# Performance work log

Measured on AMD Instinct MI355X. Metric: run time of the kernel, lower is better.

## Reference

```python
import jax, jax.numpy as jnp
import jax.lax as lax
import numpy as np

G = 128    # number of asset groups (batch)
A = 100    # n_assets per group
WIN = 10   # window_size
FD = 16    # feature_dim
H = 128    # hidden_dim


def setup_inputs() -> dict:
    key = jax.random.key(0)
    ks = jax.random.split(key, 12)
    N = G * A
    def glorot(k, shape, fan_in):
        return (jax.random.normal(k, shape, jnp.float32) / np.sqrt(fan_in)).astype(jnp.float32)
    return {
        "x": jax.random.normal(ks[0], (N, WIN, FD), jnp.float32),
        "W1": glorot(ks[1], (WIN * FD, H), WIN * FD),
        "b1": jnp.zeros((H,), jnp.float32),
        "W2": glorot(ks[2], (H, H), H),
        "b2": jnp.zeros((H,), jnp.float32),
        "W3": glorot(ks[3], (H, H), H),
        "b3": jnp.zeros((H,), jnp.float32),
        "cw1": glorot(ks[4], (H, 1, 1, 3), 3),      # conv2d_1 weight [out,in,kh,kw]
        "cb1": jnp.zeros((H,), jnp.float32),
        "cw2": glorot(ks[5], (1, H, 1, 3), 3 * H),  # conv2d_2 weight
        "cb2": jnp.zeros((1,), jnp.float32),
    }


def _corrcoef(r):
    xc = r - r.mean(axis=1, keepdims=True)
    cov = xc @ xc.T                      # divisor cancels in correlation
    d = jnp.sqrt(jnp.diag(cov))
    return cov / (d[:, None] * d[None, :])


def _conv1x3(h, w, b):
    # h: [1,C,N,H]; kernel (1,3), padding (0,1) -> NCHW conv
    out = lax.conv_general_dilated(h, w, (1, 1), ((0, 0), (1, 1)),
                                   dimension_numbers=("NCHW", "OIHW", "NCHW"))
    return out + b[None, :, None, None]


def reference(x, W1, b1, W2, b2, W3, b3, cw1, cb1, cw2, cb2):
    # block-diagonal adjacency == independent per-group adjacencies
    returns = x[:, :, -1].reshape(G, A, WIN)
    corr = jax.vmap(_corrcoef)(returns)                  # [G,A,A]
    adj = 1.0 - jnp.abs(corr) + jnp.eye(A, dtype=x.dtype)
    dinv = 1.0 / jnp.sqrt(adj.sum(axis=-1))              # [G,A]
    norm_adj = dinv[:, :, None] * adj * dinv[:, None, :] # D^-1/2 A D^-1/2

    feats = x.reshape(G, A, WIN * FD)
    h = jax.nn.relu(jnp.einsum("gij,gjf->gif", norm_adj, feats) @ W1 + b1)
    h = jax.nn.relu(jnp.einsum("gij,gjh->gih", norm_adj, h) @ W2 + b2)
    h = jax.nn.relu(jnp.einsum("gij,gjh->gih", norm_adj, h) @ W3 + b3)

    h = h.reshape(1, 1, G * A, H)                        # [1,1,N,H]
    h = jax.nn.relu(_conv1x3(h, cw1, cb1))               # [1,H,N,H]
    out = _conv1x3(h, cw2, cb2)                          # [1,1,N,H]
    return out[0, 0]                                     # [N,H]
```

## Files before the change

kernel.cpp:

```cpp
#include <hip/hip_runtime.h>

#define G   128
#define A   100
#define WIN 10
#define FD  16
#define H   128
#define NROWS (G*A)
#define K1  (WIN*FD)

typedef __attribute__((ext_vector_type(8))) short short8;
typedef __attribute__((ext_vector_type(4))) short short4v;
typedef __attribute__((ext_vector_type(4))) float floatx4;

struct BfPair { short h, l; };

__device__ inline unsigned short f2bf(float f) {
    unsigned u = __float_as_uint(f);
    u += 0x7fff + ((u >> 16) & 1);
    return (unsigned short)(u >> 16);
}
__device__ inline float bf2f(unsigned short h) {
    return __uint_as_float(((unsigned)h) << 16);
}
__device__ inline BfPair split1(float v) {
    BfPair p;
    unsigned short hb = f2bf(v);
    p.h = (short)hb;
    p.l = (short)f2bf(v - bf2f(hb));
    return p;
}

__global__ __launch_bounds__(256) void k_prep(const float* __restrict__ W1,
                                              const float* __restrict__ W2,
                                              const float* __restrict__ W3,
                                              const float* __restrict__ cw1,
                                              const float* __restrict__ cb1,
                                              const float* __restrict__ cw2,
                                              const float* __restrict__ cb2,
                                              short* __restrict__ Wh,
                                              short* __restrict__ Wl,
                                              float* __restrict__ wpack) {
    const int b = blockIdx.x, t = threadIdx.x;
    if (b < 26) {
        int l, kc, K;
        const float* Wsrc;
        if (b < 10)      { l = 0; kc = b;      K = K1; Wsrc = W1; }
        else if (b < 18) { l = 1; kc = b - 10; K = H;  Wsrc = W2; }
        else             { l = 2; kc = b - 18; K = H;  Wsrc = W3; }
        short* dh = Wh + l * 128 * 160;
        short* dl = Wl + l * 128 * 160;
        for (int e = t; e < 16 * 128; e += 256) {
            int k = kc * 16 + (e >> 7), n = e & 127;
            BfPair p = split1(Wsrc[(size_t)k * H + n]);
            dh[n * 160 + k] = p.h;
            dl[n * 160 + k] = p.l;
        }
        (void)K;
    } else {
        for (int e = t; e < 1024; e += 256) {
            int c = e >> 3, s = e & 7;
            float v;
            if (s < 3)       v = cw1[3 * c + s];
            else if (s == 3) v = cb1[c];
            else if (s < 7)  v = cw2[3 * c + (s - 4)];
            else             v = cb2[0];
            wpack[e] = v;
        }
    }
}

__global__ __launch_bounds__(256) void k_nadj(const float* __restrict__ x,
                                              short* __restrict__ Sh,
                                              short* __restrict__ Sl) {
    __shared__ float xcT[WIN][104];
    __shared__ float invn[A];
    __shared__ float adjs[A][101];
    __shared__ float dinv[A];
    const int g = blockIdx.x;
    const int t = threadIdx.x;

    for (int idx = t; idx < A * WIN; idx += 256) {
        int a = idx / WIN, w = idx % WIN;
        xcT[w][a] = x[((g * A + a) * WIN + w) * FD + (FD - 1)];
    }
    __syncthreads();
    if (t < A) {
        float m = 0.f;
        #pragma unroll
        for (int w = 0; w < WIN; w++) m += xcT[w][t];
        m *= (1.0f / WIN);
        float ss = 0.f;
        #pragma unroll
        for (int w = 0; w < WIN; w++) {
            float v = xcT[w][t] - m;
            xcT[w][t] = v;
            ss += v * v;
        }
        invn[t] = rsqrtf(ss);
    }
    __syncthreads();
    for (int tt2 = t; tt2 < 2500; tt2 += 256) {
        int ti = tt2 / 50, tj = tt2 % 50;
        int i0 = 2 * ti, j0v = 2 * tj;
        float d00 = 0.f, d01 = 0.f, d10 = 0.f, d11 = 0.f;
        #pragma unroll
        for (int w = 0; w < WIN; w++) {
            float2 xi = *(const float2*)&xcT[w][i0];
            float2 xj = *(const float2*)&xcT[w][j0v];
            d00 = fmaf(xi.x, xj.x, d00); d01 = fmaf(xi.x, xj.y, d01);
            d10 = fmaf(xi.y, xj.x, d10); d11 = fmaf(xi.y, xj.y, d11);
        }
        float ii0 = invn[i0], ii1 = invn[i0 + 1];
        float ij0 = invn[j0v], ij1 = invn[j0v + 1];
        float e = (ti == tj) ? 1.f : 0.f;
        adjs[i0][j0v]         = 1.f - fabsf(d00 * ii0 * ij0) + e;
        adjs[i0][j0v + 1]     = 1.f - fabsf(d01 * ii0 * ij1);
        adjs[i0 + 1][j0v]     = 1.f - fabsf(d10 * ii1 * ij0);
        adjs[i0 + 1][j0v + 1] = 1.f - fabsf(d11 * ii1 * ij1) + e;
    }
    __syncthreads();
    if (t < A) {
        float s = 0.f;
        for (int j = 0; j < A; j++) s += adjs[t][j];
        dinv[t] = rsqrtf(s);
    }
    __syncthreads();
    short* sh = Sh + (size_t)g * 112 * 128;
    short* sl = Sl + (size_t)g * 112 * 128;
    for (int idx = t; idx < 112 * 128; idx += 256) {
        int i = idx >> 7, k = idx & 127;
        float v = (i < A && k < A) ? dinv[i] * adjs[i][k] * dinv[k] : 0.f;
        BfPair p = split1(v);
        sh[idx] = p.h;
        sl[idx] = p.l;
    }
}

__global__ __launch_bounds__(256) void k_layer(const short* __restrict__ Sh,
                                               const short* __restrict__ Sl,
                                               const short* __restrict__ Whg,
                                               const short* __restrict__ Wlg,
                                               const float* __restrict__ X,
                                               const float* __restrict__ bias,
                                               float* __restrict__ Z, int K) {
    __shared__ short Xh[112 * 40], Xl[112 * 40];
    __shared__ short Yh[32 * 136], Yl[32 * 136];
    const int g = blockIdx.x;
    const int cbase = blockIdx.y * 32;
    const int t = threadIdx.x;
    const int w = t >> 6, lane = t & 63;
    const int quad = lane >> 4, r16 = lane & 15;
    const int nm = (w < 3) ? 2 : 1;
    const int m0 = 2 * w;

    for (int e = t; e < 384; e += 256) {
        int r = 100 + e / 32, c = e % 32;
        Xh[r * 40 + c] = 0; Xl[r * 40 + c] = 0;
    }
    for (int e = t; e < 512; e += 256) {
        int n = e >> 4, k = 112 + (e & 15);
        Yh[n * 136 + k] = 0; Yl[n * 136 + k] = 0;
    }

    floatx4 acc[2][2];
    #pragma unroll
    for (int i = 0; i < 2; i++)
        #pragma unroll
        for (int j = 0; j < 2; j++) acc[i][j] = (floatx4)0.f;

    const float* Xg = X + (size_t)g * A * K;
    const int nch = K >> 5;
    for (int c = 0; c < nch; c++) {
        const int k0 = c << 5;
        __syncthreads();
        for (int e = t; e < 400; e += 256) {
            int r = e >> 2, q = e & 3;
            const float* gp = Xg + (size_t)r * K + k0 + q * 8;
            float4 f0 = *(const float4*)gp;
            float4 f1 = *(const float4*)(gp + 4);
            float v[8] = {f0.x, f0.y, f0.z, f0.w, f1.x, f1.y, f1.z, f1.w};
            short8 hh, ll;
            #pragma unroll
            for (int i = 0; i < 8; i++) {
                BfPair p = split1(v[i]);
                hh[i] = p.h; ll[i] = p.l;
            }
            *(short8*)&Xh[r * 40 + q * 8] = hh;
            *(short8*)&Xl[r * 40 + q * 8] = ll;
        }
        __syncthreads();
        short8 bh[2], bl[2];
        #pragma unroll
        for (int nt = 0; nt < 2; nt++) {
            size_t wo = (size_t)(cbase + nt * 16 + r16) * 160 + k0 + quad * 8;
            bh[nt] = *(const short8*)(Whg + wo);
            bl[nt] = *(const short8*)(Wlg + wo);
        }
        for (int mt = 0; mt < nm; mt++) {
            int xo = ((m0 + mt) * 16 + r16) * 40 + quad * 8;
            short8 ah = *(const short8*)&Xh[xo];
            short8 al = *(const short8*)&Xl[xo];
            #pragma unroll
            for (int nt = 0; nt < 2; nt++) {
                acc[mt][nt] = __builtin_amdgcn_mfma_f32_16x16x32_bf16(ah, bh[nt], acc[mt][nt], 0, 0, 0);
                acc[mt][nt] = __builtin_amdgcn_mfma_f32_16x16x32_bf16(ah, bl[nt], acc[mt][nt], 0, 0, 0);
                acc[mt][nt] = __builtin_amdgcn_mfma_f32_16x16x32_bf16(al, bh[nt], acc[mt][nt], 0, 0, 0);
            }
        }
    }
    __syncthreads();

    for (int mt = 0; mt < nm; mt++) {
        #pragma unroll
        for (int nt = 0; nt < 2; nt++) {
            short4v yh4, yl4;
            #pragma unroll
            for (int rr = 0; rr < 4; rr++) {
                BfPair p = split1(acc[mt][nt][rr]);
                yh4[rr] = p.h; yl4[rr] = p.l;
            }
            int off = (nt * 16 + r16) * 136 + (m0 + mt) * 16 + quad * 4;
            *(short4v*)&Yh[off] = yh4;
            *(short4v*)&Yl[off] = yl4;
            acc[mt][nt] = (floatx4)0.f;
        }
    }
    __syncthreads();

    const short* Sgh = Sh + (size_t)g * 112 * 128;
    const short* Sgl = Sl + (size_t)g * 112 * 128;
    #pragma unroll
    for (int c = 0; c < 4; c++) {
        const int k0 = c << 5;
        short8 bh[2], bl[2];
        #pragma unroll
        for (int nt = 0; nt < 2; nt++) {
            int yo = (nt * 16 + r16) * 136 + k0 + quad * 8;
            bh[nt] = *(const short8*)&Yh[yo];
            bl[nt] = *(const short8*)&Yl[yo];
        }
        for (int mt = 0; mt < nm; mt++) {
            size_t so = (size_t)((m0 + mt) * 16 + r16) * 128 + k0 + quad * 8;
            short8 ah = *(const short8*)(Sgh + so);
            short8 al = *(const short8*)(Sgl + so);
            #pragma unroll
            for (int nt = 0; nt < 2; nt++) {
                acc[mt][nt] = __builtin_amdgcn_mfma_f32_16x16x32_bf16(ah, bh[nt], acc[mt][nt], 0, 0, 0);
                acc[mt][nt] = __builtin_amdgcn_mfma_f32_16x16x32_bf16(ah, bl[nt], acc[mt][nt], 0, 0, 0);
                acc[mt][nt] = __builtin_amdgcn_mfma_f32_16x16x32_bf16(al, bh[nt], acc[mt][nt], 0, 0, 0);
            }
        }
    }

    #pragma unroll
    for (int nt = 0; nt < 2; nt++) {
        float bv = bias[cbase + nt * 16 + r16];
        for (int mt = 0; mt < nm; mt++) {
            #pragma unroll
            for (int rr = 0; rr < 4; rr++) {
                int i = (m0 + mt) * 16 + quad * 4 + rr;
                if (i < A)
                    Z[((size_t)g * A + i) * H + cbase + nt * 16 + r16] =
                        fmaxf(0.f, acc[mt][nt][rr] + bv);
            }
        }
    }
}

__global__ __launch_bounds__(256) void k_conv(const float* __restrict__ h3,
                                              const float* __restrict__ wpack,
                                              float* __restrict__ out) {
    const int t = threadIdx.x;
    const int wave = t >> 6, lane = t & 63;
    const int n = blockIdx.x * 8 + wave * 2 + (lane >> 5);
    const int q = lane & 31;
    const int j0 = q * 4;
    const float* hr = h3 + (size_t)n * H;

    float hh[8];
    if (q == 0) {
        float4 a  = *(const float4*)(hr);
        float2 b2 = *(const float2*)(hr + 4);
        hh[0] = 0.f;  hh[1] = 0.f;  hh[2] = a.x;  hh[3] = a.y;
        hh[4] = a.z;  hh[5] = a.w;  hh[6] = b2.x; hh[7] = b2.y;
    } else if (q == 31) {
        float2 b2 = *(const float2*)(hr + 122);
        float4 a  = *(const float4*)(hr + 124);
        hh[0] = b2.x; hh[1] = b2.y; hh[2] = a.x;  hh[3] = a.y;
        hh[4] = a.z;  hh[5] = a.w;  hh[6] = 0.f;  hh[7] = 0.f;
    } else {
        float4 a  = *(const float4*)(hr + j0 - 2);
        float4 b4 = *(const float4*)(hr + j0 + 2);
        hh[0] = a.x;  hh[1] = a.y;  hh[2] = a.z;  hh[3] = a.w;
        hh[4] = b4.x; hh[5] = b4.y; hh[6] = b4.z; hh[7] = b4.w;
    }
    const float mlo = (q == 0)  ? 0.f : 1.f;
    const float mhi = (q == 31) ? 0.f : 1.f;

    float acc[4] = {0.f, 0.f, 0.f, 0.f};
    #pragma unroll 8
    for (int c = 0; c < H; c++) {
        const float* wp = wpack + c * 8;
        float w0 = wp[0], w1 = wp[1], w2 = wp[2], b = wp[3];
        float v0 = wp[4], v1 = wp[5], v2 = wp[6];
        float tt[6];
        #pragma unroll
        for (int m = 0; m < 6; m++)
            tt[m] = fmaxf(0.f, fmaf(w2, hh[m + 2],
                               fmaf(w1, hh[m + 1],
                               fmaf(w0, hh[m], b))));
        tt[0] *= mlo;
        tt[5] *= mhi;
        #pragma unroll
        for (int p = 0; p < 4; p++)
            acc[p] = fmaf(v0, tt[p],
                     fmaf(v1, tt[p + 1],
                     fmaf(v2, tt[p + 2], acc[p])));
    }
    const float c2b = wpack[7];
    *(float4*)(out + (size_t)n * H + j0) =
        make_float4(acc[0] + c2b, acc[1] + c2b, acc[2] + c2b, acc[3] + c2b);
}

extern "C" void kernel_launch(void* const* d_in, const int* in_sizes, int n_in,
                              void* d_out, int out_size, void* d_ws, size_t ws_size,
                              hipStream_t stream) {
    const float* x   = (const float*)d_in[0];
    const float* W1  = (const float*)d_in[1];
    const float* b1  = (const float*)d_in[2];
    const float* W2  = (const float*)d_in[3];
    const float* b2  = (const float*)d_in[4];
    const float* W3  = (const float*)d_in[5];
    const float* b3  = (const float*)d_in[6];
    const float* cw1 = (const float*)d_in[7];
    const float* cb1 = (const float*)d_in[8];
    const float* cw2 = (const float*)d_in[9];
    const float* cb2 = (const float*)d_in[10];
    float* out = (float*)d_out;

    short* Sh = (short*)d_ws;
    short* Sl = Sh + (size_t)G * 112 * 128;
    short* Wh = Sl + (size_t)G * 112 * 128;
    short* Wl = Wh + 3 * 128 * 160;
    float* wpack = (float*)(Wl + 3 * 128 * 160);
    float* bufA  = wpack + 1024;
    float* bufB  = bufA + (size_t)NROWS * H;

    k_prep<<<27, 256, 0, stream>>>(W1, W2, W3, cw1, cb1, cw2, cb2, Wh, Wl, wpack);
    k_nadj<<<G, 256, 0, stream>>>(x, Sh, Sl);

    k_layer<<<dim3(G, 4), 256, 0, stream>>>(Sh, Sl, Wh,             Wl,             x,    b1, bufA, K1);
    k_layer<<<dim3(G, 4), 256, 0, stream>>>(Sh, Sl, Wh + 128 * 160, Wl + 128 * 160, bufA, b2, bufB, H);
    k_layer<<<dim3(G, 4), 256, 0, stream>>>(Sh, Sl, Wh + 256 * 160, Wl + 256 * 160, bufB, b3, bufA, H);

    k_conv<<<NROWS / 8, 256, 0, stream>>>(bufA, wpack, out);
}
```

Measured before the change: 200.6 us.

## Split GCN layer into global X@W and S@Y kernels with bf16-pair intermediates

Each fused per-group layer kernel becomes two kernels. k_ymm computes X@W over 16-row tiles across all groups and writes transposed Y as bf16 hi/lo into a padded per-group buffer. k_smm then multiplies the normalized adjacency by Y and applies bias and ReLU, storing bf16 hi/lo (fp32 on the last layer). The aim is to stop recomputing the X tile split for every column block, to avoid LDS round trips and barriers, and to store intermediates in a smaller bf16 form. The conv kernel now stages its weights in LDS itself and handles two rows per thread, and the wpack prep path is gone. The cost is more kernel launches, 64-thread blocks with lower occupancy per block, and scattered 2-byte global stores of Y.

```diff
diff --git a/kernel.cpp b/kernel.cpp
--- a/kernel.cpp
+++ b/kernel.cpp
@@ -9,7 +9,6 @@
 #define K1  (WIN*FD)
 
 typedef __attribute__((ext_vector_type(8))) short short8;
-typedef __attribute__((ext_vector_type(4))) short short4v;
 typedef __attribute__((ext_vector_type(4))) float floatx4;
 
 struct BfPair { short h, l; };
@@ -33,51 +32,46 @@
 __global__ __launch_bounds__(256) void k_prep(const float* __restrict__ W1,
                                               const float* __restrict__ W2,
                                               const float* __restrict__ W3,
-                                              const float* __restrict__ cw1,
-                                              const float* __restrict__ cb1,
-                                              const float* __restrict__ cw2,
-                                              const float* __restrict__ cb2,
                                               short* __restrict__ Wh,
-                                              short* __restrict__ Wl,
-                                              float* __restrict__ wpack) {
+                                              short* __restrict__ Wl) {
     const int b = blockIdx.x, t = threadIdx.x;
-    if (b < 26) {
-        int l, kc, K;
-        const float* Wsrc;
-        if (b < 10)      { l = 0; kc = b;      K = K1; Wsrc = W1; }
-        else if (b < 18) { l = 1; kc = b - 10; K = H;  Wsrc = W2; }
-        else             { l = 2; kc = b - 18; K = H;  Wsrc = W3; }
-        short* dh = Wh + l * 128 * 160;
-        short* dl = Wl + l * 128 * 160;
-        for (int e = t; e < 16 * 128; e += 256) {
-            int k = kc * 16 + (e >> 7), n = e & 127;
-            BfPair p = split1(Wsrc[(size_t)k * H + n]);
-            dh[n * 160 + k] = p.h;
-            dl[n * 160 + k] = p.l;
-        }
-        (void)K;
-    } else {
-        for (int e = t; e < 1024; e += 256) {
-            int c = e >> 3, s = e & 7;
-            float v;
-            if (s < 3)       v = cw1[3 * c + s];
-            else if (s == 3) v = cb1[c];
-            else if (s < 7)  v = cw2[3 * c + (s - 4)];
-            else             v = cb2[0];
-            wpack[e] = v;
-        }
+    int l, kc;
+    const float* Wsrc;
+    if (b < 10)      { l = 0; kc = b;      Wsrc = W1; }
+    else if (b < 18) { l = 1; kc = b - 10; Wsrc = W2; }
+    else             { l = 2; kc = b - 18; Wsrc = W3; }
+    short* dh = Wh + l * 128 * 160;
+    short* dl = Wl + l * 128 * 160;
+    for (int e = t; e < 16 * 128; e += 256) {
+        int k = kc * 16 + (e >> 7), n = e & 127;
+        BfPair p = split1(Wsrc[(size_t)k * H + n]);
+        dh[n * 160 + k] = p.h;
+        dl[n * 160 + k] = p.l;
     }
 }
 
 __global__ __launch_bounds__(256) void k_nadj(const float* __restrict__ x,
                                               short* __restrict__ Sh,
-                                              short* __restrict__ Sl) {
+                                              short* __restrict__ Sl,
+                                              short* __restrict__ Yh,
+                                              short* __restrict__ Yl) {
     __shared__ float xcT[WIN][104];
     __shared__ float invn[A];
     __shared__ float adjs[A][101];
     __shared__ float dinv[A];
     const int g = blockIdx.x;
     const int t = threadIdx.x;
+
+    {
+        short8 z8 = (short8)0;
+        short* ygh = Yh + (size_t)g * 128 * 128;
+        short* ygl = Yl + (size_t)g * 128 * 128;
+        for (int e = t; e < 512; e += 256) {
+            int n = e >> 2, j = 96 + (e & 3) * 8;
+            *(short8*)(ygh + n * 128 + j) = z8;
+            *(short8*)(ygl + n * 128 + j) = z8;
+        }
+    }
 
     for (int idx = t; idx < A * WIN; idx += 256) {
         int a = idx / WIN, w = idx % WIN;
@@ -136,148 +130,129 @@
     }
 }
 
-__global__ __launch_bounds__(256) void k_layer(const short* __restrict__ Sh,
-                                               const short* __restrict__ Sl,
-                                               const short* __restrict__ Whg,
-                                               const short* __restrict__ Wlg,
-                                               const float* __restrict__ X,
-                                               const float* __restrict__ bias,
-                                               float* __restrict__ Z, int K) {
-    __shared__ short Xh[112 * 40], Xl[112 * 40];
-    __shared__ short Yh[32 * 136], Yl[32 * 136];
-    const int g = blockIdx.x;
-    const int cbase = blockIdx.y * 32;
-    const int t = threadIdx.x;
-    const int w = t >> 6, lane = t & 63;
-    const int quad = lane >> 4, r16 = lane & 15;
-    const int nm = (w < 3) ? 2 : 1;
-    const int m0 = 2 * w;
-
-    for (int e = t; e < 384; e += 256) {
-        int r = 100 + e / 32, c = e % 32;
-        Xh[r * 40 + c] = 0; Xl[r * 40 + c] = 0;
-    }
-    for (int e = t; e < 512; e += 256) {
-        int n = e >> 4, k = 112 + (e & 15);
-        Yh[n * 136 + k] = 0; Yl[n * 136 + k] = 0;
-    }
-
-    floatx4 acc[2][2];
-    #pragma unroll
-    for (int i = 0; i < 2; i++)
-        #pragma unroll
-        for (int j = 0; j < 2; j++) acc[i][j] = (floatx4)0.f;
-
-    const float* Xg = X + (size_t)g * A * K;
+__global__ __launch_bounds__(64) void k_ymm(const float* __restrict__ X1,
+                                            const short* __restrict__ Zh,
+                                            const short* __restrict__ Zl,
+                                            const short* __restrict__ Whg,
+                                            const short* __restrict__ Wlg,
+                                            short* __restrict__ Yh,
+                                            short* __restrict__ Yl, int K) {
+    const int mtile = blockIdx.x;
+    const int lane = threadIdx.x;
+    const int r16 = lane & 15, quad = lane >> 4;
+    const int row = mtile * 16 + r16;
+
+    floatx4 acc[8];
+    #pragma unroll
+    for (int nt = 0; nt < 8; nt++) acc[nt] = (floatx4)0.f;
+
     const int nch = K >> 5;
     for (int c = 0; c < nch; c++) {
         const int k0 = c << 5;
-        __syncthreads();
-        for (int e = t; e < 400; e += 256) {
-            int r = e >> 2, q = e & 3;
-            const float* gp = Xg + (size_t)r * K + k0 + q * 8;
+        short8 ah, al;
+        if (K == K1) {
+            const float* gp = X1 + (size_t)row * K1 + k0 + quad * 8;
             float4 f0 = *(const float4*)gp;
             float4 f1 = *(const float4*)(gp + 4);
             float v[8] = {f0.x, f0.y, f0.z, f0.w, f1.x, f1.y, f1.z, f1.w};
-            short8 hh, ll;
             #pragma unroll
             for (int i = 0; i < 8; i++) {
                 BfPair p = split1(v[i]);
-                hh[i] = p.h; ll[i] = p.l;
+                ah[i] = p.h; al[i] = p.l;
             }
-            *(short8*)&Xh[r * 40 + q * 8] = hh;
-            *(short8*)&Xl[r * 40 + q * 8] = ll;
-        }
-        __syncthreads();
-        short8 bh[2], bl[2];
-        #pragma unroll
-        for (int nt = 0; nt < 2; nt++) {
-            size_t wo = (size_t)(cbase + nt * 16 + r16) * 160 + k0 + quad * 8;
-            bh[nt] = *(const short8*)(Whg + wo);
-            bl[nt] = *(const short8*)(Wlg + wo);
-        }
-        for (int mt = 0; mt < nm; mt++) {
-            int xo = ((m0 + mt) * 16 + r16) * 40 + quad * 8;
-            short8 ah = *(const short8*)&Xh[xo];
-            short8 al = *(const short8*)&Xl[xo];
-            #pragma unroll
-            for (int nt = 0; nt < 2; nt++) {
-                acc[mt][nt] = __builtin_amdgcn_mfma_f32_16x16x32_bf16(ah, bh[nt], acc[mt][nt], 0, 0, 0);
-                acc[mt][nt] = __builtin_amdgcn_mfma_f32_16x16x32_bf16(ah, bl[nt], acc[mt][nt], 0, 0, 0);
-                acc[mt][nt] = __builtin_amdgcn_mfma_f32_16x16x32_bf16(al, bh[nt], acc[mt][nt], 0, 0, 0);
-            }
-        }
-    }
-    __syncthreads();
-
-    for (int mt = 0; mt < nm; mt++) {
-        #pragma unroll
-        for (int nt = 0; nt < 2; nt++) {
-            short4v yh4, yl4;
-            #pragma unroll
-            for (int rr = 0; rr < 4; rr++) {
-                BfPair p = split1(acc[mt][nt][rr]);
-                yh4[rr] = p.h; yl4[rr] = p.l;
-            }
-            int off = (nt * 16 + r16) * 136 + (m0 + mt) * 16 + quad * 4;
-            *(short4v*)&Yh[off] = yh4;
-            *(short4v*)&Yl[off] = yl4;
-            acc[mt][nt] = (floatx4)0.f;
-        }
-    }
-    __syncthreads();
-
-    const short* Sgh = Sh + (size_t)g * 112 * 128;
-    const short* Sgl = Sl + (size_t)g * 112 * 128;
+        } else {
+            ah = *(const short8*)(Zh + (size_t)row * H + k0 + quad * 8);
+            al = *(const short8*)(Zl + (size_t)row * H + k0 + quad * 8);
+        }
+        #pragma unroll
+        for (int nt = 0; nt < 8; nt++) {
+            size_t wo = (size_t)(nt * 16 + r16) * 160 + k0 + quad * 8;
+            short8 bh = *(const short8*)(Whg + wo);
+            short8 bl = *(const short8*)(Wlg + wo);
+            acc[nt] = __builtin_amdgcn_mfma_f32_16x16x32_bf16(ah, bh, acc[nt], 0, 0, 0);
+            acc[nt] = __builtin_amdgcn_mfma_f32_16x16x32_bf16(ah, bl, acc[nt], 0, 0, 0);
+            acc[nt] = __builtin_amdgcn_mfma_f32_16x16x32_bf16(al, bh, acc[nt], 0, 0, 0);
+        }
+    }
+
+    #pragma unroll
+    for (int rr = 0; rr < 4; rr++) {
+        int rm = mtile * 16 + quad * 4 + rr;
+        int g = rm / 100, j = rm - g * 100;
+        size_t base = (size_t)g * 128 * 128 + j;
+        #pragma unroll
+        for (int nt = 0; nt < 8; nt++) {
+            BfPair p = split1(acc[nt][rr]);
+            size_t o = base + (size_t)(nt * 16 + r16) * 128;
+            Yh[o] = p.h;
+            Yl[o] = p.l;
+        }
+    }
+}
+
+__global__ __launch_bounds__(64) void k_smm(const short* __restrict__ Sh,
+                                            const short* __restrict__ Sl,
+                                            const short* __restrict__ Yh,
+                                            const short* __restrict__ Yl,
+                                            const float* __restrict__ bias,
+                                            short* __restrict__ Zh,
+                                            short* __restrict__ Zl,
+                                            float* __restrict__ Zf, int last) {
+    const int g = blockIdx.x, mt = blockIdx.y;
+    const int lane = threadIdx.x;
+    const int r16 = lane & 15, quad = lane >> 4;
+
+    floatx4 acc[8];
+    #pragma unroll
+    for (int nt = 0; nt < 8; nt++) acc[nt] = (floatx4)0.f;
+
+    const short* sgh = Sh + ((size_t)g * 112 + mt * 16 + r16) * 128;
+    const short* sgl = Sl + ((size_t)g * 112 + mt * 16 + r16) * 128;
+    const short* ygh = Yh + (size_t)g * 128 * 128;
+    const short* ygl = Yl + (size_t)g * 128 * 128;
+
     #pragma unroll
     for (int c = 0; c < 4; c++) {
         const int k0 = c << 5;
-        short8 bh[2], bl[2];
-        #pragma unroll
-        for (int nt = 0; nt < 2; nt++) {
-            int yo = (nt * 16 + r16) * 136 + k0 + quad * 8;
-            bh[nt] = *(const short8*)&Yh[yo];
-            bl[nt] = *(const short8*)&Yl[yo];
-        }
-        for (int mt = 0; mt < nm; mt++) {
-            size_t so = (size_t)((m0 + mt) * 16 + r16) * 128 + k0 + quad * 8;
-            short8 ah = *(const short8*)(Sgh + so);
-            short8 al = *(const short8*)(Sgl + so);
-            #pragma unroll
-            for (int nt = 0; nt < 2; nt++) {
-                acc[mt][nt] = __builtin_amdgcn_mfma_f32_16x16x32_bf16(ah, bh[nt], acc[mt][nt], 0, 0, 0);
-                acc[mt][nt] = __builtin_amdgcn_mfma_f32_16x16x32_bf16(ah, bl[nt], acc[mt][nt], 0, 0, 0);
-                acc[mt][nt] = __builtin_amdgcn_mfma_f32_16x16x32_bf16(al, bh[nt], acc[mt][nt], 0, 0, 0);
+        short8 ah = *(const short8*)(sgh + k0 + quad * 8);
+        short8 al = *(const short8*)(sgl + k0 + quad * 8);
+        #pragma unroll
+        for (int nt = 0; nt < 8; nt++) {
+            size_t yo = (size_t)(nt * 16 + r16) * 128 + k0 + quad * 8;
+            short8 bh = *(const short8*)(ygh + yo);
+            short8 bl = *(const short8*)(ygl + yo);
+            acc[nt] = __builtin_amdgcn_mfma_f32_16x16x32_bf16(ah, bh, acc[nt], 0, 0, 0);
+            acc[nt] = __builtin_amdgcn_mfma_f32_16x16x32_bf16(ah, bl, acc[nt], 0, 0, 0);
+            acc[nt] = __builtin_amdgcn_mfma_f32_16x16x32_bf16(al, bh, acc[nt], 0, 0, 0);
+        }
+    }
+
+    float bv[8];
+    #pragma unroll
+    for (int nt = 0; nt < 8; nt++) bv[nt] = bias[nt * 16 + r16];
+
+    #pragma unroll
+    for (int nt = 0; nt < 8; nt++) {
+        int col = nt * 16 + r16;
+        #pragma unroll
+        for (int rr = 0; rr < 4; rr++) {
+            int i = mt * 16 + quad * 4 + rr;
+            if (i < A) {
+                size_t row = (size_t)g * A + i;
+                float v = fmaxf(0.f, acc[nt][rr] + bv[nt]);
+                if (last) {
+                    Zf[row * H + col] = v;
+                } else {
+                    BfPair p = split1(v);
+                    Zh[row * H + col] = p.h;
+                    Zl[row * H + col] = p.l;
+                }
             }
         }
     }
-
-    #pragma unroll
-    for (int nt = 0; nt < 2; nt++) {
-        float bv = bias[cbase + nt * 16 + r16];
-        for (int mt = 0; mt < nm; mt++) {
-            #pragma unroll
-            for (int rr = 0; rr < 4; rr++) {
-                int i = (m0 + mt) * 16 + quad * 4 + rr;
-                if (i < A)
-                    Z[((size_t)g * A + i) * H + cbase + nt * 16 + r16] =
-                        fmaxf(0.f, acc[mt][nt][rr] + bv);
-            }
-        }
-    }
-}
-
-__global__ __launch_bounds__(256) void k_conv(const float* __restrict__ h3,
-                                              const float* __restrict__ wpack,
-                                              float* __restrict__ out) {
-    const int t = threadIdx.x;
-    const int wave = t >> 6, lane = t & 63;
-    const int n = blockIdx.x * 8 + wave * 2 + (lane >> 5);
-    const int q = lane & 31;
-    const int j0 = q * 4;
-    const float* hr = h3 + (size_t)n * H;
-
-    float hh[8];
+}
+
+__device__ inline void load_hh(const float* hr, int q, int j0, float* hh) {
     if (q == 0) {
         float4 a  = *(const float4*)(hr);
         float2 b2 = *(const float2*)(hr + 4);
@@ -294,32 +269,67 @@
         hh[0] = a.x;  hh[1] = a.y;  hh[2] = a.z;  hh[3] = a.w;
         hh[4] = b4.x; hh[5] = b4.y; hh[6] = b4.z; hh[7] = b4.w;
     }
+}
+
+__global__ __launch_bounds__(256) void k_conv(const float* __restrict__ h3,
+                                              const float* __restrict__ cw1,
+                                              const float* __restrict__ cb1,
+                                              const float* __restrict__ cw2,
+                                              const float* __restrict__ cb2,
+                                              float* __restrict__ out) {
+    __shared__ float wbuf[H][8];
+    const int t = threadIdx.x;
+    if (t < H) {
+        *(float4*)&wbuf[t][0] = make_float4(cw1[3 * t], cw1[3 * t + 1], cw1[3 * t + 2], cb1[t]);
+        *(float4*)&wbuf[t][4] = make_float4(cw2[3 * t], cw2[3 * t + 1], cw2[3 * t + 2], 0.f);
+    }
+    __syncthreads();
+
+    const int wave = t >> 6, lane = t & 63;
+    const int s = lane >> 5, q = lane & 31;
+    const int j0 = q * 4;
+    const int base = blockIdx.x * 16 + wave * 4;
+    const int ra = base + s;
+    const int rb = ra + 2;
+    const float* hra = h3 + (size_t)ra * H;
+    const float* hrb = h3 + (size_t)rb * H;
+
+    float hha[8], hhb[8];
+    load_hh(hra, q, j0, hha);
+    load_hh(hrb, q, j0, hhb);
+
     const float mlo = (q == 0)  ? 0.f : 1.f;
     const float mhi = (q == 31) ? 0.f : 1.f;
 
-    float acc[4] = {0.f, 0.f, 0.f, 0.f};
-    #pragma unroll 8
+    float acca[4] = {0.f, 0.f, 0.f, 0.f};
+    float accb[4] = {0.f, 0.f, 0.f, 0.f};
+    #pragma unroll 2
     for (int c = 0; c < H; c++) {
-        const float* wp = wpack + c * 8;
-        float w0 = wp[0], w1 = wp[1], w2 = wp[2], b = wp[3];
-        float v0 = wp[4], v1 = wp[5], v2 = wp[6];
-        float tt[6];
-        #pragma unroll
-        for (int m = 0; m < 6; m++)
-            tt[m] = fmaxf(0.f, fmaf(w2, hh[m + 2],
-                               fmaf(w1, hh[m + 1],
-                               fmaf(w0, hh[m], b))));
-        tt[0] *= mlo;
-        tt[5] *= mhi;
-        #pragma unroll
-        for (int p = 0; p < 4; p++)
-            acc[p] = fmaf(v0, tt[p],
-                     fmaf(v1, tt[p + 1],
-                     fmaf(v2, tt[p + 2], acc[p])));
-    }
-    const float c2b = wpack[7];
-    *(float4*)(out + (size_t)n * H + j0) =
-        make_float4(acc[0] + c2b, acc[1] + c2b, acc[2] + c2b, acc[3] + c2b);
+        float4 wA = *(const float4*)&wbuf[c][0];
+        float4 wB = *(const float4*)&wbuf[c][4];
+        float ta[6], tb[6];
+        #pragma unroll
+        for (int m = 0; m < 6; m++) {
+            ta[m] = fmaxf(0.f, fmaf(wA.z, hha[m + 2],
+                               fmaf(wA.y, hha[m + 1],
+                               fmaf(wA.x, hha[m], wA.w))));
+            tb[m] = fmaxf(0.f, fmaf(wA.z, hhb[m + 2],
+                               fmaf(wA.y, hhb[m + 1],
+                               fmaf(wA.x, hhb[m], wA.w))));
+        }
+        ta[0] *= mlo; ta[5] *= mhi;
+        tb[0] *= mlo; tb[5] *= mhi;
+        #pragma unroll
+        for (int p = 0; p < 4; p++) {
+            acca[p] = fmaf(wB.x, ta[p], fmaf(wB.y, ta[p + 1], fmaf(wB.z, ta[p + 2], acca[p])));
+            accb[p] = fmaf(wB.x, tb[p], fmaf(wB.y, tb[p + 1], fmaf(wB.z, tb[p + 2], accb[p])));
+        }
+    }
+    const float c2b = cb2[0];
+    *(float4*)(out + (size_t)ra * H + j0) =
+        make_float4(acca[0] + c2b, acca[1] + c2b, acca[2] + c2b, acca[3] + c2b);
+    *(float4*)(out + (size_t)rb * H + j0) =
+        make_float4(accb[0] + c2b, accb[1] + c2b, accb[2] + c2b, accb[3] + c2b);
 }
 
 extern "C" void kernel_launch(void* const* d_in, const int* in_sizes, int n_in,
@@ -342,16 +352,21 @@
     short* Sl = Sh + (size_t)G * 112 * 128;
     short* Wh = Sl + (size_t)G * 112 * 128;
     short* Wl = Wh + 3 * 128 * 160;
-    float* wpack = (float*)(Wl + 3 * 128 * 160);
-    float* bufA  = wpack + 1024;
-    float* bufB  = bufA + (size_t)NROWS * H;
-
-    k_prep<<<27, 256, 0, stream>>>(W1, W2, W3, cw1, cb1, cw2, cb2, Wh, Wl, wpack);
-    k_nadj<<<G, 256, 0, stream>>>(x, Sh, Sl);
-
-    k_layer<<<dim3(G, 4), 256, 0, stream>>>(Sh, Sl, Wh,             Wl,             x,    b1, bufA, K1);
-    k_layer<<<dim3(G, 4), 256, 0, stream>>>(Sh, Sl, Wh + 128 * 160, Wl + 128 * 160, bufA, b2, bufB, H);
-    k_layer<<<dim3(G, 4), 256, 0, stream>>>(Sh, Sl, Wh + 256 * 160, Wl + 256 * 160, bufB, b3, bufA, H);
-
-    k_conv<<<NROWS / 8, 256, 0, stream>>>(bufA, wpack, out);
-}
+    short* Yh = Wl + 3 * 128 * 160;
+    short* Yl = Yh + (size_t)G * 128 * 128;
+    short* Zh = Yl + (size_t)G * 128 * 128;
+    short* Zl = Zh + (size_t)NROWS * H;
+    float* h3f = (float*)Zh;
+
+    k_prep<<<26, 256, 0, stream>>>(W1, W2, W3, Wh, Wl);
+    k_nadj<<<G, 256, 0, stream>>>(x, Sh, Sl, Yh, Yl);
+
+    k_ymm<<<NROWS / 16, 64, 0, stream>>>(x, Zh, Zl, Wh, Wl, Yh, Yl, K1);
+    k_smm<<<dim3(G, 7), 64, 0, stream>>>(Sh, Sl, Yh, Yl, b1, Zh, Zl, h3f, 0);
+    k_ymm<<<NROWS / 16, 64, 0, stream>>>(x, Zh, Zl, Wh + 128 * 160, Wl + 128 * 160, Yh, Yl, H);
+    k_smm<<<dim3(G, 7), 64, 0, stream>>>(Sh, Sl, Yh, Yl, b2, Zh, Zl, h3f, 0);
+    k_ymm<<<NROWS / 16, 64, 0, stream>>>(x, Zh, Zl, Wh + 256 * 160, Wl + 256 * 160, Yh, Yl, H);
+    k_smm<<<dim3(G, 7), 64, 0, stream>>>(Sh, Sl, Yh, Yl, b3, Zh, Zl, h3f, 1);
+
+    k_conv<<<NROWS / 16, 256, 0, stream>>>(h3f, cw1, cb1, cw2, cb2, out);
+}
```

New measurement: 282.4 us. +40.8%, slower.
